# Kernel tuning notes

Measured on AMD Instinct MI355X. Metric: run time of the kernel, lower is better.

Reference implementation:

```python
import jax, jax.numpy as jnp
import numpy as np

TEMP = 1.0
EPS = 1e-12  # F.normalize eps

N, D, C, Q = 128, 512, 8192, 32768


def setup_inputs() -> dict:
    key = jax.random.key(0)
    ks = jax.random.split(key, 8)
    feat_queue = jax.random.normal(ks[4], (Q, D), dtype=jnp.float32)
    # queue holds previously-enqueued (normalized) old embeddings
    feat_queue = feat_queue / jnp.maximum(jnp.linalg.norm(feat_queue, axis=1, keepdims=True), EPS)
    return {
        "old_embeds": jax.random.normal(ks[0], (N, D), dtype=jnp.float32),
        "old_logits": jax.random.normal(ks[1], (N, C), dtype=jnp.float32),
        "new_embeds": jax.random.normal(ks[2], (N, D), dtype=jnp.float32),
        "new_logits": jax.random.normal(ks[3], (N, C), dtype=jnp.float32),
        "labels": jax.random.randint(ks[5], (N,), 0, C, dtype=jnp.int64) if jax.config.jax_enable_x64 else jax.random.randint(ks[5], (N,), 0, C, dtype=jnp.int32),
        "feat_queue": feat_queue,
        "logit_queue": jax.random.normal(ks[6], (Q, C), dtype=jnp.float32),
        "queue_labels": jax.random.randint(ks[7], (Q,), 0, C, dtype=jnp.int32),
        "header": 1000,
    }


def _masked_contrastive(scores, mask, weight):
    # scores: [N, Q]; replicate torch: subtract detached row max, then log-softmax denom
    s = scores - jax.lax.stop_gradient(jnp.max(scores, axis=1, keepdims=True))
    log_prob = s - jnp.log(jnp.sum(jnp.exp(s), axis=1, keepdims=True))
    mean_log_prob_pos = jnp.sum(mask * log_prob * weight, axis=1) / jnp.sum(mask, axis=1)
    return -jnp.mean(mean_log_prob_pos)


def reference(old_embeds, old_logits, new_embeds, new_logits, labels,
              feat_queue, logit_queue, queue_labels, header):
    n = old_embeds.shape[0]
    q = feat_queue.shape[0]
    # vectorized circular queue update (replaces per-sample python loop)
    idx = (header + jnp.arange(n)) % q
    feat_queue = feat_queue.at[idx].set(old_embeds)
    logit_queue = logit_queue.at[idx].set(old_logits)
    queue_labels = queue_labels.at[idx].set(labels.astype(queue_labels.dtype))

    new_e = new_embeds / jnp.maximum(
        jnp.linalg.norm(new_embeds, axis=1, keepdims=True), EPS)

    old_outputs = old_embeds @ feat_queue.T           # [N, Q]
    weight = 0.5 * (old_outputs + 1.0)
    mask = (queue_labels[None, :] == labels[:, None]).astype(new_e.dtype)

    outputs = (new_e @ feat_queue.T) / TEMP           # [N, Q]
    l1_loss = _masked_contrastive(outputs, mask, weight)

    logits = (new_logits @ logit_queue.T) / TEMP      # [N, Q]
    l2_loss = _masked_contrastive(logits, mask, weight)
    return (l1_loss, l2_loss)
```

## Files before the change

### kernel.cpp

```cpp
#include <hip/hip_runtime.h>

#define Q 32768
#define NR 128
#define D 512
#define C 8192

typedef __attribute__((ext_vector_type(8))) short bf16x8;
typedef __attribute__((ext_vector_type(4))) float f32x4;

__device__ __forceinline__ unsigned short f2bf(float f) {
  union { float f; unsigned u; } v; v.f = f;
  return (unsigned short)((v.u + 0x7fffu + ((v.u >> 16) & 1u)) >> 16);
}

__global__ __launch_bounds__(256) void prep_kernel(
    const float* __restrict__ old_embeds, const float* __restrict__ old_logits,
    const float* __restrict__ new_embeds, const float* __restrict__ new_logits,
    const int* __restrict__ labels, float* __restrict__ feat_queue,
    float* __restrict__ logit_queue, int* __restrict__ queue_labels,
    const int* __restrict__ headerp, unsigned short* __restrict__ A1,
    unsigned short* __restrict__ A2) {
  const int b = blockIdx.x, t = threadIdx.x;
  const int header = *headerp;
  if (b < 1024) {
    int base = b * 1024 + t * 4;
    int row = base >> 13, col = base & (C - 1);
    int qrow = (header + row) % Q;
    *(float4*)(logit_queue + (size_t)qrow * C + col) =
        *(const float4*)(old_logits + base);
  } else if (b < 2048) {
    int base = (b - 1024) * 1024 + t * 4;
    float4 v = *(const float4*)(new_logits + base);
    short4 p;
    p.x = (short)f2bf(v.x); p.y = (short)f2bf(v.y);
    p.z = (short)f2bf(v.z); p.w = (short)f2bf(v.w);
    *(short4*)(A2 + base) = p;
  } else if (b < 2112) {
    int base = (b - 2048) * 1024 + t * 4;
    int row = base >> 9, col = base & (D - 1);
    int qrow = (header + row) % Q;
    *(float4*)(feat_queue + (size_t)qrow * D + col) =
        *(const float4*)(old_embeds + base);
  } else if (b == 2112) {
    if (t < NR) queue_labels[(header + t) % Q] = labels[t];
  } else {
    int r = b - 2113;
    float x0 = new_embeds[r * D + t];
    float x1 = new_embeds[r * D + t + 256];
    float s = x0 * x0 + x1 * x1;
    #pragma unroll
    for (int off = 32; off; off >>= 1) s += __shfl_down(s, off);
    __shared__ float red[5];
    if ((t & 63) == 0) red[t >> 6] = s;
    __syncthreads();
    if (t == 0)
      red[4] = 1.0f / fmaxf(sqrtf(red[0] + red[1] + red[2] + red[3]), 1e-12f);
    __syncthreads();
    float sc = red[4];
    A1[r * D + t] = f2bf(x0 * sc);
    A1[r * D + t + 256] = f2bf(x1 * sc);
  }
}

template <int K>
__global__ __launch_bounds__(256) void gemm_scores(
    const unsigned short* __restrict__ A, const float* __restrict__ B,
    float* __restrict__ S) {
  __shared__ unsigned short As[128 * 64];
  __shared__ unsigned short Bs[64 * 64];
  const int t = threadIdx.x;
  const int lane = t & 63, w = t >> 6;
  const int l15 = lane & 15, l4 = lane >> 4;
  const int n0 = blockIdx.x * 64;
  f32x4 acc[2][4] = {};

  for (int k0 = 0; k0 < K; k0 += 64) {
    #pragma unroll
    for (int rep = 0; rep < 4; rep++) {
      int c = w * 256 + rep * 64 + lane;
      const unsigned short* gp = A + (size_t)(c >> 3) * K + k0 + (c & 7) * 8;
      __builtin_amdgcn_global_load_lds(
          (__attribute__((address_space(1))) void*)gp,
          (__attribute__((address_space(3))) void*)(As + (w * 256 + rep * 64) * 8),
          16, 0, 0);
    }
    float4 bv[4];
    #pragma unroll
    for (int rep = 0; rep < 4; rep++) {
      int c = rep * 256 + t;
      bv[rep] = *(const float4*)(B + (size_t)(n0 + (c >> 4)) * K + k0 + (c & 15) * 4);
    }
    #pragma unroll
    for (int rep = 0; rep < 4; rep++) {
      int c = rep * 256 + t;
      short4 p;
      p.x = (short)f2bf(bv[rep].x); p.y = (short)f2bf(bv[rep].y);
      p.z = (short)f2bf(bv[rep].z); p.w = (short)f2bf(bv[rep].w);
      *(short4*)&Bs[(c >> 4) * 64 + (c & 15) * 4] = p;
    }
    __syncthreads();
    #pragma unroll
    for (int kk = 0; kk < 64; kk += 32) {
      bf16x8 a0 = *(const bf16x8*)&As[(w * 32 + l15) * 64 + kk + l4 * 8];
      bf16x8 a1 = *(const bf16x8*)&As[(w * 32 + 16 + l15) * 64 + kk + l4 * 8];
      #pragma unroll
      for (int tn = 0; tn < 4; tn++) {
        bf16x8 bb = *(const bf16x8*)&Bs[(tn * 16 + l15) * 64 + kk + l4 * 8];
        acc[0][tn] = __builtin_amdgcn_mfma_f32_16x16x32_bf16(a0, bb, acc[0][tn], 0, 0, 0);
        acc[1][tn] = __builtin_amdgcn_mfma_f32_16x16x32_bf16(a1, bb, acc[1][tn], 0, 0, 0);
      }
    }
    __syncthreads();
  }
  #pragma unroll
  for (int tm = 0; tm < 2; tm++)
    #pragma unroll
    for (int tn = 0; tn < 4; tn++)
      #pragma unroll
      for (int r = 0; r < 4; r++) {
        int row = w * 32 + tm * 16 + l4 * 4 + r;
        int col = n0 + tn * 16 + l15;
        S[(size_t)row * Q + col] = acc[tm][tn][r];
      }
}

__global__ __launch_bounds__(256) void row_reduce(
    const float* __restrict__ S1, const float* __restrict__ S2,
    const int* __restrict__ labels, const int* __restrict__ queue_labels,
    const float* __restrict__ old_embeds, const float* __restrict__ feat_queue,
    float* __restrict__ terms) {
  const int i = blockIdx.x, t = threadIdx.x;
  const int lab = labels[i];
  const float* oe = old_embeds + (size_t)i * D;
  float m1 = -__builtin_inff(), z1 = 0.f, m2 = -__builtin_inff(), z2 = 0.f;
  float a1 = 0.f, a2 = 0.f, bw = 0.f, cn = 0.f;
  for (int j = t; j < Q; j += 256) {
    float s1 = S1[(size_t)i * Q + j];
    float s2 = S2[(size_t)i * Q + j];
    if (s1 > m1) { z1 = z1 * __expf(m1 - s1) + 1.f; m1 = s1; }
    else z1 += __expf(s1 - m1);
    if (s2 > m2) { z2 = z2 * __expf(m2 - s2) + 1.f; m2 = s2; }
    else z2 += __expf(s2 - m2);
    if (queue_labels[j] == lab) {
      const float* fq = feat_queue + (size_t)j * D;
      float dot = 0.f;
      #pragma unroll 4
      for (int k = 0; k < D; k += 4) {
        float4 a = *(const float4*)(oe + k);
        float4 b4 = *(const float4*)(fq + k);
        dot += a.x * b4.x + a.y * b4.y + a.z * b4.z + a.w * b4.w;
      }
      float wgt = 0.5f * (dot + 1.f);
      a1 += wgt * s1; a2 += wgt * s2; bw += wgt; cn += 1.f;
    }
  }
  __shared__ float sm1[256], sz1[256], sm2[256], sz2[256];
  __shared__ float sa1[256], sa2[256], sbw[256], scn[256];
  sm1[t] = m1; sz1[t] = z1; sm2[t] = m2; sz2[t] = z2;
  sa1[t] = a1; sa2[t] = a2; sbw[t] = bw; scn[t] = cn;
  __syncthreads();
  if (t == 0) {
    float M1 = -__builtin_inff(), Z1 = 0.f, M2 = -__builtin_inff(), Z2 = 0.f;
    float A1s = 0.f, A2s = 0.f, BW = 0.f, CN = 0.f;
    for (int k = 0; k < 256; k++) {
      float mk = sm1[k];
      if (mk > M1) { Z1 = Z1 * __expf(M1 - mk) + sz1[k]; M1 = mk; }
      else Z1 += sz1[k] * __expf(mk - M1);
      mk = sm2[k];
      if (mk > M2) { Z2 = Z2 * __expf(M2 - mk) + sz2[k]; M2 = mk; }
      else Z2 += sz2[k] * __expf(mk - M2);
      A1s += sa1[k]; A2s += sa2[k]; BW += sbw[k]; CN += scn[k];
    }
    float lse1 = M1 + __logf(Z1);
    float lse2 = M2 + __logf(Z2);
    terms[i * 2] = (A1s - lse1 * BW) / CN;
    terms[i * 2 + 1] = (A2s - lse2 * BW) / CN;
  }
}

__global__ __launch_bounds__(128) void finalize_kernel(
    const float* __restrict__ terms, float* __restrict__ out) {
  int t = threadIdx.x;
  float t1 = terms[t * 2], t2 = terms[t * 2 + 1];
  #pragma unroll
  for (int off = 32; off; off >>= 1) {
    t1 += __shfl_down(t1, off);
    t2 += __shfl_down(t2, off);
  }
  __shared__ float r[4];
  if ((t & 63) == 0) { r[(t >> 6) * 2] = t1; r[(t >> 6) * 2 + 1] = t2; }
  __syncthreads();
  if (t == 0) {
    out[0] = -(r[0] + r[2]) / 128.0f;
    out[1] = -(r[1] + r[3]) / 128.0f;
  }
}

extern "C" void kernel_launch(void* const* d_in, const int* in_sizes, int n_in,
                              void* d_out, int out_size, void* d_ws, size_t ws_size,
                              hipStream_t stream) {
  const float* old_embeds = (const float*)d_in[0];
  const float* old_logits = (const float*)d_in[1];
  const float* new_embeds = (const float*)d_in[2];
  const float* new_logits = (const float*)d_in[3];
  const int* labels = (const int*)d_in[4];
  float* feat_queue = (float*)d_in[5];
  float* logit_queue = (float*)d_in[6];
  int* queue_labels = (int*)d_in[7];
  const int* headerp = (const int*)d_in[8];

  char* ws = (char*)d_ws;
  unsigned short* A1 = (unsigned short*)ws;
  unsigned short* A2 = (unsigned short*)(ws + (128 * 512 * 2));
  float* S1 = (float*)(ws + 128 * 512 * 2 + 128 * 8192 * 2);
  float* S2 = S1 + (size_t)NR * Q;
  float* terms = S2 + (size_t)NR * Q;

  prep_kernel<<<2241, 256, 0, stream>>>(old_embeds, old_logits, new_embeds,
                                        new_logits, labels, feat_queue,
                                        logit_queue, queue_labels, headerp,
                                        A1, A2);
  gemm_scores<512><<<Q / 64, 256, 0, stream>>>(A1, feat_queue, S1);
  gemm_scores<8192><<<Q / 64, 256, 0, stream>>>(A2, logit_queue, S2);
  row_reduce<<<NR, 256, 0, stream>>>(S1, S2, labels, queue_labels, old_embeds,
                                     feat_queue, terms);
  finalize_kernel<<<1, 128, 0, stream>>>(terms, (float*)d_out);
}
```

Measured before the change: 1.766 ms.

## Fuse softmax/mask reductions into GEMM epilogue and double-buffer GEMM tiles

The GEMM kernels now compute per-block partial online-softmax statistics (max, sum-exp, weighted positive sums, counts) directly from the accumulators, so the two 128x32768 score matrices are no longer written or re-read. A small combine kernel merges the per-block partials per row. The K loop is also double-buffered in LDS, prefetching the next A/B tile while MFMAs run on the current one. This costs extra LDS and epilogue work, and the masked dot products are recomputed in each GEMM block.

Result: no change. 1.751 ms (-0.9%).

```diff
diff --git a/kernel.cpp b/kernel.cpp
--- a/kernel.cpp
+++ b/kernel.cpp
@@ -4,6 +4,7 @@
 #define NR 128
 #define D 512
 #define C 8192
+#define NBLK (Q / 64)
 
 typedef __attribute__((ext_vector_type(8))) short bf16x8;
 typedef __attribute__((ext_vector_type(4))) float f32x4;
@@ -62,33 +63,36 @@
   }
 }
 
-template <int K>
-__global__ __launch_bounds__(256) void gemm_scores(
+template <int K, bool WW>
+__global__ __launch_bounds__(256) void gemm_fused(
     const unsigned short* __restrict__ A, const float* __restrict__ B,
-    float* __restrict__ S) {
-  __shared__ unsigned short As[128 * 64];
-  __shared__ unsigned short Bs[64 * 64];
+    const int* __restrict__ labels, const int* __restrict__ queue_labels,
+    const float* __restrict__ old_embeds, const float* __restrict__ feat_queue,
+    float* __restrict__ Pm, float* __restrict__ Pz, float* __restrict__ Pa,
+    float* __restrict__ Pbw, float* __restrict__ Pcn) {
+  __shared__ unsigned short As[2][128 * 64];
+  __shared__ unsigned short Bs[2][64 * 64];
   const int t = threadIdx.x;
   const int lane = t & 63, w = t >> 6;
   const int l15 = lane & 15, l4 = lane >> 4;
   const int n0 = blockIdx.x * 64;
   f32x4 acc[2][4] = {};
 
-  for (int k0 = 0; k0 < K; k0 += 64) {
-    #pragma unroll
-    for (int rep = 0; rep < 4; rep++) {
-      int c = w * 256 + rep * 64 + lane;
-      const unsigned short* gp = A + (size_t)(c >> 3) * K + k0 + (c & 7) * 8;
-      __builtin_amdgcn_global_load_lds(
-          (__attribute__((address_space(1))) void*)gp,
-          (__attribute__((address_space(3))) void*)(As + (w * 256 + rep * 64) * 8),
-          16, 0, 0);
-    }
+  #pragma unroll
+  for (int rep = 0; rep < 4; rep++) {
+    int c = w * 256 + rep * 64 + lane;
+    const unsigned short* gp = A + (size_t)(c >> 3) * K + (c & 7) * 8;
+    __builtin_amdgcn_global_load_lds(
+        (__attribute__((address_space(1))) void*)gp,
+        (__attribute__((address_space(3))) void*)(&As[0][0] + (w * 256 + rep * 64) * 8),
+        16, 0, 0);
+  }
+  {
     float4 bv[4];
     #pragma unroll
     for (int rep = 0; rep < 4; rep++) {
       int c = rep * 256 + t;
-      bv[rep] = *(const float4*)(B + (size_t)(n0 + (c >> 4)) * K + k0 + (c & 15) * 4);
+      bv[rep] = *(const float4*)(B + (size_t)(n0 + (c >> 4)) * K + (c & 15) * 4);
     }
     #pragma unroll
     for (int rep = 0; rep < 4; rep++) {
@@ -96,85 +100,141 @@
       short4 p;
       p.x = (short)f2bf(bv[rep].x); p.y = (short)f2bf(bv[rep].y);
       p.z = (short)f2bf(bv[rep].z); p.w = (short)f2bf(bv[rep].w);
-      *(short4*)&Bs[(c >> 4) * 64 + (c & 15) * 4] = p;
-    }
-    __syncthreads();
+      *(short4*)&Bs[0][(c >> 4) * 64 + (c & 15) * 4] = p;
+    }
+  }
+  __syncthreads();
+
+  for (int k0 = 0; k0 < K; k0 += 64) {
+    const int buf = (k0 >> 6) & 1, nbuf = buf ^ 1;
+    const bool more = (k0 + 64 < K);
+    float4 bv[4];
+    if (more) {
+      #pragma unroll
+      for (int rep = 0; rep < 4; rep++) {
+        int c = w * 256 + rep * 64 + lane;
+        const unsigned short* gp = A + (size_t)(c >> 3) * K + (k0 + 64) + (c & 7) * 8;
+        __builtin_amdgcn_global_load_lds(
+            (__attribute__((address_space(1))) void*)gp,
+            (__attribute__((address_space(3))) void*)(&As[nbuf][0] + (w * 256 + rep * 64) * 8),
+            16, 0, 0);
+      }
+      #pragma unroll
+      for (int rep = 0; rep < 4; rep++) {
+        int c = rep * 256 + t;
+        bv[rep] = *(const float4*)(B + (size_t)(n0 + (c >> 4)) * K + (k0 + 64) + (c & 15) * 4);
+      }
+    }
     #pragma unroll
     for (int kk = 0; kk < 64; kk += 32) {
-      bf16x8 a0 = *(const bf16x8*)&As[(w * 32 + l15) * 64 + kk + l4 * 8];
-      bf16x8 a1 = *(const bf16x8*)&As[(w * 32 + 16 + l15) * 64 + kk + l4 * 8];
+      bf16x8 a0 = *(const bf16x8*)&As[buf][(w * 32 + l15) * 64 + kk + l4 * 8];
+      bf16x8 a1 = *(const bf16x8*)&As[buf][(w * 32 + 16 + l15) * 64 + kk + l4 * 8];
       #pragma unroll
       for (int tn = 0; tn < 4; tn++) {
-        bf16x8 bb = *(const bf16x8*)&Bs[(tn * 16 + l15) * 64 + kk + l4 * 8];
+        bf16x8 bb = *(const bf16x8*)&Bs[buf][(tn * 16 + l15) * 64 + kk + l4 * 8];
         acc[0][tn] = __builtin_amdgcn_mfma_f32_16x16x32_bf16(a0, bb, acc[0][tn], 0, 0, 0);
         acc[1][tn] = __builtin_amdgcn_mfma_f32_16x16x32_bf16(a1, bb, acc[1][tn], 0, 0, 0);
       }
     }
+    if (more) {
+      #pragma unroll
+      for (int rep = 0; rep < 4; rep++) {
+        int c = rep * 256 + t;
+        short4 p;
+        p.x = (short)f2bf(bv[rep].x); p.y = (short)f2bf(bv[rep].y);
+        p.z = (short)f2bf(bv[rep].z); p.w = (short)f2bf(bv[rep].w);
+        *(short4*)&Bs[nbuf][(c >> 4) * 64 + (c & 15) * 4] = p;
+      }
+    }
     __syncthreads();
   }
-  #pragma unroll
-  for (int tm = 0; tm < 2; tm++)
-    #pragma unroll
-    for (int tn = 0; tn < 4; tn++)
-      #pragma unroll
-      for (int r = 0; r < 4; r++) {
-        int row = w * 32 + tm * 16 + l4 * 4 + r;
-        int col = n0 + tn * 16 + l15;
-        S[(size_t)row * Q + col] = acc[tm][tn][r];
-      }
-}
-
-__global__ __launch_bounds__(256) void row_reduce(
-    const float* __restrict__ S1, const float* __restrict__ S2,
-    const int* __restrict__ labels, const int* __restrict__ queue_labels,
-    const float* __restrict__ old_embeds, const float* __restrict__ feat_queue,
+
+  int qlab[4];
+  #pragma unroll
+  for (int tn = 0; tn < 4; tn++) qlab[tn] = queue_labels[n0 + tn * 16 + l15];
+
+  #pragma unroll
+  for (int tm = 0; tm < 2; tm++) {
+    #pragma unroll
+    for (int r = 0; r < 4; r++) {
+      const int row = w * 32 + tm * 16 + l4 * 4 + r;
+      const int lab = labels[row];
+      float m = acc[tm][0][r];
+      #pragma unroll
+      for (int tn = 1; tn < 4; tn++) m = fmaxf(m, acc[tm][tn][r]);
+      float z = 0.f, a = 0.f, bwv = 0.f, cnv = 0.f;
+      #pragma unroll
+      for (int tn = 0; tn < 4; tn++) {
+        float s = acc[tm][tn][r];
+        z += __expf(s - m);
+        if (qlab[tn] == lab) {
+          const float* oe = old_embeds + (size_t)row * D;
+          const float* fq = feat_queue + (size_t)(n0 + tn * 16 + l15) * D;
+          float dot = 0.f;
+          #pragma unroll 4
+          for (int k = 0; k < D; k += 4) {
+            float4 av = *(const float4*)(oe + k);
+            float4 bv4 = *(const float4*)(fq + k);
+            dot += av.x * bv4.x + av.y * bv4.y + av.z * bv4.z + av.w * bv4.w;
+          }
+          float wt = 0.5f * (dot + 1.f);
+          a += wt * s; bwv += wt; cnv += 1.f;
+        }
+      }
+      #pragma unroll
+      for (int d = 1; d < 16; d <<= 1) {
+        float mo = __shfl_xor(m, d), zo = __shfl_xor(z, d);
+        float M = fmaxf(m, mo);
+        z = z * __expf(m - M) + zo * __expf(mo - M);
+        m = M;
+        a += __shfl_xor(a, d);
+        if (WW) { bwv += __shfl_xor(bwv, d); cnv += __shfl_xor(cnv, d); }
+      }
+      if (l15 == 0) {
+        const size_t idx = (size_t)row * NBLK + blockIdx.x;
+        Pm[idx] = m; Pz[idx] = z; Pa[idx] = a;
+        if (WW) { Pbw[idx] = bwv; Pcn[idx] = cnv; }
+      }
+    }
+  }
+}
+
+__global__ __launch_bounds__(64) void combine_kernel(
+    const float* __restrict__ Pm1, const float* __restrict__ Pz1,
+    const float* __restrict__ Pa1, const float* __restrict__ Pm2,
+    const float* __restrict__ Pz2, const float* __restrict__ Pa2,
+    const float* __restrict__ Pbw, const float* __restrict__ Pcn,
     float* __restrict__ terms) {
-  const int i = blockIdx.x, t = threadIdx.x;
-  const int lab = labels[i];
-  const float* oe = old_embeds + (size_t)i * D;
-  float m1 = -__builtin_inff(), z1 = 0.f, m2 = -__builtin_inff(), z2 = 0.f;
-  float a1 = 0.f, a2 = 0.f, bw = 0.f, cn = 0.f;
-  for (int j = t; j < Q; j += 256) {
-    float s1 = S1[(size_t)i * Q + j];
-    float s2 = S2[(size_t)i * Q + j];
-    if (s1 > m1) { z1 = z1 * __expf(m1 - s1) + 1.f; m1 = s1; }
-    else z1 += __expf(s1 - m1);
-    if (s2 > m2) { z2 = z2 * __expf(m2 - s2) + 1.f; m2 = s2; }
-    else z2 += __expf(s2 - m2);
-    if (queue_labels[j] == lab) {
-      const float* fq = feat_queue + (size_t)j * D;
-      float dot = 0.f;
-      #pragma unroll 4
-      for (int k = 0; k < D; k += 4) {
-        float4 a = *(const float4*)(oe + k);
-        float4 b4 = *(const float4*)(fq + k);
-        dot += a.x * b4.x + a.y * b4.y + a.z * b4.z + a.w * b4.w;
-      }
-      float wgt = 0.5f * (dot + 1.f);
-      a1 += wgt * s1; a2 += wgt * s2; bw += wgt; cn += 1.f;
-    }
-  }
-  __shared__ float sm1[256], sz1[256], sm2[256], sz2[256];
-  __shared__ float sa1[256], sa2[256], sbw[256], scn[256];
-  sm1[t] = m1; sz1[t] = z1; sm2[t] = m2; sz2[t] = z2;
-  sa1[t] = a1; sa2[t] = a2; sbw[t] = bw; scn[t] = cn;
-  __syncthreads();
-  if (t == 0) {
-    float M1 = -__builtin_inff(), Z1 = 0.f, M2 = -__builtin_inff(), Z2 = 0.f;
-    float A1s = 0.f, A2s = 0.f, BW = 0.f, CN = 0.f;
-    for (int k = 0; k < 256; k++) {
-      float mk = sm1[k];
-      if (mk > M1) { Z1 = Z1 * __expf(M1 - mk) + sz1[k]; M1 = mk; }
-      else Z1 += sz1[k] * __expf(mk - M1);
-      mk = sm2[k];
-      if (mk > M2) { Z2 = Z2 * __expf(M2 - mk) + sz2[k]; M2 = mk; }
-      else Z2 += sz2[k] * __expf(mk - M2);
-      A1s += sa1[k]; A2s += sa2[k]; BW += sbw[k]; CN += scn[k];
-    }
-    float lse1 = M1 + __logf(Z1);
-    float lse2 = M2 + __logf(Z2);
-    terms[i * 2] = (A1s - lse1 * BW) / CN;
-    terms[i * 2 + 1] = (A2s - lse2 * BW) / CN;
+  const int row = blockIdx.x, l = threadIdx.x;
+  float m1 = -__builtin_inff(), z1 = 0.f, a1 = 0.f;
+  float m2 = -__builtin_inff(), z2 = 0.f, a2 = 0.f;
+  float bw = 0.f, cn = 0.f;
+  for (int b = l; b < NBLK; b += 64) {
+    const size_t idx = (size_t)row * NBLK + b;
+    float mo = Pm1[idx], zo = Pz1[idx];
+    float M = fmaxf(m1, mo);
+    z1 = z1 * __expf(m1 - M) + zo * __expf(mo - M); m1 = M;
+    a1 += Pa1[idx];
+    mo = Pm2[idx]; zo = Pz2[idx];
+    M = fmaxf(m2, mo);
+    z2 = z2 * __expf(m2 - M) + zo * __expf(mo - M); m2 = M;
+    a2 += Pa2[idx];
+    bw += Pbw[idx]; cn += Pcn[idx];
+  }
+  #pragma unroll
+  for (int d = 1; d < 64; d <<= 1) {
+    float mo = __shfl_xor(m1, d), zo = __shfl_xor(z1, d);
+    float M = fmaxf(m1, mo);
+    z1 = z1 * __expf(m1 - M) + zo * __expf(mo - M); m1 = M;
+    mo = __shfl_xor(m2, d); zo = __shfl_xor(z2, d);
+    M = fmaxf(m2, mo);
+    z2 = z2 * __expf(m2 - M) + zo * __expf(mo - M); m2 = M;
+    a1 += __shfl_xor(a1, d); a2 += __shfl_xor(a2, d);
+    bw += __shfl_xor(bw, d); cn += __shfl_xor(cn, d);
+  }
+  if (l == 0) {
+    terms[row * 2]     = (a1 - (m1 + __logf(z1)) * bw) / cn;
+    terms[row * 2 + 1] = (a2 - (m2 + __logf(z2)) * bw) / cn;
   }
 }
 
@@ -211,18 +271,25 @@
 
   char* ws = (char*)d_ws;
   unsigned short* A1 = (unsigned short*)ws;
-  unsigned short* A2 = (unsigned short*)(ws + (128 * 512 * 2));
-  float* S1 = (float*)(ws + 128 * 512 * 2 + 128 * 8192 * 2);
-  float* S2 = S1 + (size_t)NR * Q;
-  float* terms = S2 + (size_t)NR * Q;
+  unsigned short* A2 = (unsigned short*)(ws + 128 * 512 * 2);
+  float* P = (float*)(ws + 128 * 512 * 2 + 128 * 8192 * 2);
+  const size_t PSZ = (size_t)NR * NBLK;
+  float* Pm1 = P;            float* Pz1 = P + PSZ;      float* Pa1 = P + 2 * PSZ;
+  float* Pm2 = P + 3 * PSZ;  float* Pz2 = P + 4 * PSZ;  float* Pa2 = P + 5 * PSZ;
+  float* Pbw = P + 6 * PSZ;  float* Pcn = P + 7 * PSZ;
+  float* terms = P + 8 * PSZ;
 
   prep_kernel<<<2241, 256, 0, stream>>>(old_embeds, old_logits, new_embeds,
                                         new_logits, labels, feat_queue,
                                         logit_queue, queue_labels, headerp,
                                         A1, A2);
-  gemm_scores<512><<<Q / 64, 256, 0, stream>>>(A1, feat_queue, S1);
-  gemm_scores<8192><<<Q / 64, 256, 0, stream>>>(A2, logit_queue, S2);
-  row_reduce<<<NR, 256, 0, stream>>>(S1, S2, labels, queue_labels, old_embeds,
-                                     feat_queue, terms);
+  gemm_fused<512, true><<<NBLK, 256, 0, stream>>>(
+      A1, feat_queue, labels, queue_labels, old_embeds, feat_queue,
+      Pm1, Pz1, Pa1, Pbw, Pcn);
+  gemm_fused<8192, false><<<NBLK, 256, 0, stream>>>(
+      A2, logit_queue, labels, queue_labels, old_embeds, feat_queue,
+      Pm2, Pz2, Pa2, nullptr, nullptr);
+  combine_kernel<<<NR, 64, 0, stream>>>(Pm1, Pz1, Pa1, Pm2, Pz2, Pa2,
+                                        Pbw, Pcn, terms);
   finalize_kernel<<<1, 128, 0, stream>>>(terms, (float*)d_out);
 }
```
